# Optimization experiments

Measured on AMD Instinct MI355X. Metric: run time of the kernel, lower is better.

Reference implementation:

```python
import jax, jax.numpy as jnp
import numpy as np

BL = 512              # block length (init kwarg bl)
HALF = BL // 2
WIN = BL + 2 * HALF   # window width seen by each query block
Q_DIM = K_DIM = V_DIM = 256
R1 = R2 = R3 = 2
CQ, CK, CV = Q_DIM // R1, K_DIM // R2, V_DIM // R3


def setup_inputs() -> dict:
    key = jax.random.key(0)
    ks = jax.random.split(key, 9)
    B, L = 1, 131072
    def w(k, shape, fan):
        return (jax.random.normal(k, shape, jnp.float32) / np.float32(np.sqrt(fan)))
    return {
        "x1": jax.random.normal(ks[0], (B, Q_DIM, L), jnp.float32),
        "mask": jnp.ones((B, 1, L), jnp.float32),
        "Wq": w(ks[1], (CQ, Q_DIM), Q_DIM), "bq": jnp.zeros((CQ,), jnp.float32),
        "Wk": w(ks[2], (CK, K_DIM), K_DIM), "bk": jnp.zeros((CK,), jnp.float32),
        "Wv": w(ks[3], (CV, V_DIM), V_DIM), "bv": jnp.zeros((CV,), jnp.float32),
        "Wo": w(ks[4], (V_DIM, CV), CV),   "bo": jnp.zeros((V_DIM,), jnp.float32),
    }


def conv1x1(W, b, x):
    # nn.Conv1d(kernel_size=1): (B, Cin, L) -> (B, Cout, L)
    return jnp.einsum('oc,bcl->bol', W, x) + b[None, :, None]


def _sliding_window_att(q, k, v, mask):
    B, cq, L = q.shape
    cv = v.shape[1]
    nb = L // BL  # L chosen divisible by BL (remainder-pad branch is a no-op)
    # per-frame padding mask, (B,1,L)
    pm = jnp.broadcast_to(mask[:, 0:1, :], (B, 1, L))
    # blocked queries: (B*nb, cq, BL)
    qb = q.reshape(B, cq, nb, BL).transpose(0, 2, 1, 3).reshape(B * nb, cq, BL)
    # pad k / v / mask by HALF zeros on both sides, then take overlapping windows
    kp = jnp.pad(k, ((0, 0), (0, 0), (HALF, HALF)))
    vp = jnp.pad(v, ((0, 0), (0, 0), (HALF, HALF)))
    mp = jnp.pad(pm, ((0, 0), (0, 0), (HALF, HALF)))
    idx = np.arange(nb)[:, None] * BL + np.arange(WIN)[None, :]
    kb = kp[:, :, idx].transpose(0, 2, 1, 3).reshape(B * nb, -1, WIN)
    vb = vp[:, :, idx].transpose(0, 2, 1, 3).reshape(B * nb, -1, WIN)
    mb = mp[:, :, idx].transpose(0, 2, 1, 3).reshape(B * nb, 1, WIN)
    # construct_window_mask: loop sets window_mask[:, :, i:i+BL] = 1 for i in [0,BL),
    # whose union is columns [0, 2*BL-1) for ALL rows (faithful to the given code).
    wm = (jnp.arange(WIN) < (2 * BL - 1)).astype(q.dtype)[None, None, :]
    fm = wm * mb  # final mask, broadcasts over the BL query rows
    # scalar_dot_att with log-mask trick
    energy = jnp.einsum('ncl,ncw->nlw', qb, kb) / np.float32(np.sqrt(cq))
    att = jax.nn.softmax(energy + jnp.log(fm + 1e-6), axis=-1) * fm
    out = jnp.einsum('ncw,nlw->ncl', vb, att)  # (B*nb, cv, BL)
    return out, nb, cv


def reference(x1, mask, Wq, bq, Wk, bk, Wv, bv, Wo, bo):
    B, _, L = x1.shape
    q = conv1x1(Wq, bq, x1)
    k = conv1x1(Wk, bk, x1)
    v = conv1x1(Wv, bv, x1)
    out, nb, cv = _sliding_window_att(q, k, v, mask)
    out = conv1x1(Wo, bo, jax.nn.relu(out))  # (B*nb, V_DIM, BL)
    out = out.reshape(B, nb, V_DIM, BL).transpose(0, 2, 1, 3).reshape(B, V_DIM, nb * BL)
    out = out[:, :, :L]
    return out * mask[:, 0:1, :]
```

## Files before the change

kernel.cpp:

```cpp
#include <hip/hip_runtime.h>
#include <math.h>

#define LTOT 131072

typedef unsigned short u16;
typedef unsigned int   u32;
typedef __attribute__((ext_vector_type(8))) short bf16x8;
typedef __attribute__((ext_vector_type(4))) short bf16x4;
typedef __attribute__((ext_vector_type(4))) float f32x4;

__device__ __forceinline__ u16 f2b(float f) {
  union { float f; u32 u; } v; v.f = f;
  u32 r = v.u + 0x7fffu + ((v.u >> 16) & 1u);
  return (u16)(r >> 16);
}

__device__ __forceinline__ u32 cvt_pk(float lo, float hi) {
  u32 r;
  asm("v_cvt_pk_bf16_f32 %0, %1, %2" : "=v"(r) : "v"(lo), "v"(hi));
  return r;
}

__device__ __forceinline__ bf16x8 pack_bp(const f32x4 a, const f32x4 b) {
  union { u32 w[4]; bf16x8 v; } u;
  u.w[0] = cvt_pk(a[0], a[1]);
  u.w[1] = cvt_pk(a[2], a[3]);
  u.w[2] = cvt_pk(b[0], b[1]);
  u.w[3] = cvt_pk(b[2], b[3]);
  return u.v;
}

__device__ __forceinline__ int sxt_addr(int row, int g) {
  return (row << 8) + (((g) ^ (row & 7)) << 3);
}

__global__ __launch_bounds__(512) void k_qkv(
    const float* __restrict__ x1,
    const float* __restrict__ Wq, const float* __restrict__ bq,
    const float* __restrict__ Wk, const float* __restrict__ bk,
    const float* __restrict__ Wv, const float* __restrict__ bv,
    const float* __restrict__ Wo,
    u16* __restrict__ scratch, u16* __restrict__ WoB)
{
  __shared__ __align__(16) u16 sXT[128 * 256];

  const int tid  = threadIdx.x;
  const int lane = tid & 63;
  const int wv   = tid >> 6;
  const int lr   = lane & 15;
  const int lg   = lane >> 4;
  const int l0   = blockIdx.x << 7;

  {
    const int cl = (tid & 63) << 1;
    const int kq = tid >> 6;
#pragma unroll
    for (int k8 = 0; k8 < 4; ++k8) {
      const int k0 = kq * 32 + k8 * 8;
      float2 v[8];
#pragma unroll
      for (int j = 0; j < 8; ++j)
        v[j] = *reinterpret_cast<const float2*>(x1 + (size_t)(k0 + j) * LTOT + l0 + cl);
      union { u16 h[8]; bf16x8 b; } p0, p1;
#pragma unroll
      for (int j = 0; j < 8; ++j) {
        p0.h[j] = f2b(v[j].x);
        p1.h[j] = f2b(v[j].y);
      }
      const int g = k0 >> 3;
      *reinterpret_cast<bf16x8*>(&sXT[sxt_addr(cl,     g)]) = p0.b;
      *reinterpret_cast<bf16x8*>(&sXT[sxt_addr(cl + 1, g)]) = p1.b;
    }
  }

  if (blockIdx.x == 0) {
    for (int idx = tid; idx < 32768; idx += 512) WoB[idx] = f2b(Wo[idx]);
  }
  __syncthreads();

  const float rs = 0.1275174468f;

#pragma unroll
  for (int wb = 0; wb < 2; ++wb) {
    const float* Wsel = wb ? Wk : Wq;
    const float* bsel = wb ? bk : bq;
    const int c = (wv << 4) + lr;

    bf16x8 bw[8];
    {
      const float* wrow = Wsel + (size_t)c * 256 + (lg << 3);
#pragma unroll
      for (int kc = 0; kc < 8; ++kc) {
        float4 wa = *reinterpret_cast<const float4*>(wrow + kc * 32);
        float4 wc = *reinterpret_cast<const float4*>(wrow + kc * 32 + 4);
        union { u16 h[8]; bf16x8 b; } u;
        u.h[0] = f2b(wa.x); u.h[1] = f2b(wa.y); u.h[2] = f2b(wa.z); u.h[3] = f2b(wa.w);
        u.h[4] = f2b(wc.x); u.h[5] = f2b(wc.y); u.h[6] = f2b(wc.z); u.h[7] = f2b(wc.w);
        bw[kc] = u.b;
      }
    }

    f32x4 acc[8];
#pragma unroll
    for (int mt = 0; mt < 8; ++mt) acc[mt] = (f32x4){0.f, 0.f, 0.f, 0.f};
#pragma unroll
    for (int kc = 0; kc < 8; ++kc) {
      const int g = (kc << 2) + lg;
#pragma unroll
      for (int mt = 0; mt < 8; ++mt) {
        bf16x8 a = *reinterpret_cast<const bf16x8*>(&sXT[sxt_addr((mt << 4) + lr, g)]);
        acc[mt] = __builtin_amdgcn_mfma_f32_16x16x32_bf16(bw[kc], a, acc[mt], 0, 0, 0);
      }
    }

    const int c0 = (wv << 4) + (lg << 2);
    float4 b4 = *reinterpret_cast<const float4*>(bsel + c0);
    const float bb[4] = {b4.x, b4.y, b4.z, b4.w};
    const float scale = wb ? 1.f : rs;
    u16* dst = scratch + (size_t)wb * 128 * LTOT;
#pragma unroll
    for (int mt = 0; mt < 8; ++mt) {
      const int l = l0 + (mt << 4) + lr;
      union { u16 h[4]; uint2 v; } s;
#pragma unroll
      for (int r = 0; r < 4; ++r)
        s.h[r] = f2b((acc[mt][r] + bb[r]) * scale);
      *reinterpret_cast<uint2*>(dst + (size_t)l * 128 + c0) = s.v;
    }
  }

  {
    const int c = (wv << 4) + lr;
    bf16x8 aw[8];
    {
      const float* wrow = Wv + (size_t)c * 256 + (lg << 3);
#pragma unroll
      for (int kc = 0; kc < 8; ++kc) {
        float4 wa = *reinterpret_cast<const float4*>(wrow + kc * 32);
        float4 wc = *reinterpret_cast<const float4*>(wrow + kc * 32 + 4);
        union { u16 h[8]; bf16x8 b; } u;
        u.h[0] = f2b(wa.x); u.h[1] = f2b(wa.y); u.h[2] = f2b(wa.z); u.h[3] = f2b(wa.w);
        u.h[4] = f2b(wc.x); u.h[5] = f2b(wc.y); u.h[6] = f2b(wc.z); u.h[7] = f2b(wc.w);
        aw[kc] = u.b;
      }
    }

    f32x4 acc[8];
#pragma unroll
    for (int nt = 0; nt < 8; ++nt) acc[nt] = (f32x4){0.f, 0.f, 0.f, 0.f};
#pragma unroll
    for (int kc = 0; kc < 8; ++kc) {
      const int g = (kc << 2) + lg;
#pragma unroll
      for (int nt = 0; nt < 8; ++nt) {
        bf16x8 b = *reinterpret_cast<const bf16x8*>(&sXT[sxt_addr((nt << 4) + lr, g)]);
        acc[nt] = __builtin_amdgcn_mfma_f32_16x16x32_bf16(b, aw[kc], acc[nt], 0, 0, 0);
      }
    }

    const float bias = bv[c];
    u16* dstv = scratch + (size_t)256 * LTOT + (size_t)c * LTOT;
#pragma unroll
    for (int nt = 0; nt < 8; ++nt) {
      const int p0 = l0 + (nt << 4) + (lg << 2);
      union { u16 h[4]; uint2 v; } s;
#pragma unroll
      for (int r = 0; r < 4; ++r)
        s.h[r] = f2b(acc[nt][r] + bias);
      *reinterpret_cast<uint2*>(dstv + p0) = s.v;
    }
  }
}

__global__ __launch_bounds__(512, 4) void k_attn(
    const u16* __restrict__ scratch,
    const float* __restrict__ mask,
    u16* __restrict__ attT)
{
  __shared__ __align__(16) unsigned char smem[44032];
  u16*   sKT = (u16*)smem;
  u16*   sV  = (u16*)(smem + 17408);
  float* sLF = (float*)(smem + 35840);
  float* sFM = (float*)(smem + 39936);

  const int tid  = threadIdx.x;
  const int lane = tid & 63;
  const int wv   = tid >> 6;
  const int lr   = lane & 15;
  const int lg   = lane >> 4;
  const int lid  = ((int)blockIdx.x & 7) * 128 + ((int)blockIdx.x >> 3);
  const int lq0  = lid << 7;
  const int nblk = lq0 >> 9;
  const int p_base = nblk * 512 - 256;
  const int wq0  = lq0 + wv * 16;

  const u16* QT = scratch;
  const u16* KT = scratch + (size_t)128 * LTOT;
  const u16* Vp = scratch + (size_t)256 * LTOT;

  for (int idx = tid; idx < 1024; idx += 512) {
    int p = p_base + idx;
    float fmv = 0.f;
    if (idx < 1023 && (unsigned)p < (unsigned)LTOT) fmv = mask[p];
    sFM[idx] = fmv;
    sLF[idx] = log2f(fmv + 1e-6f);
  }

  bf16x8 aQ[4];
#pragma unroll
  for (int kc = 0; kc < 4; ++kc)
    aQ[kc] = *reinterpret_cast<const bf16x8*>(
        QT + (size_t)(wq0 + lr) * 128 + kc * 32 + (lg << 3));

  float m_run = -INFINITY;
  f32x4 d4 = (f32x4){0.f, 0.f, 0.f, 0.f};
  f32x4 accO[8];
#pragma unroll
  for (int cm = 0; cm < 8; ++cm) accO[cm] = (f32x4){0.f, 0.f, 0.f, 0.f};

  uint4 rk[2], rv[2];
  {
    const int p0 = p_base;
#pragma unroll
    for (int j = 0; j < 2; ++j) {
      int idx = tid + j * 512;
      int row = idx >> 4, ch = (idx & 15) << 3;
      int p = p0 + row;
      rk[j] = make_uint4(0u, 0u, 0u, 0u);
      if ((unsigned)p < (unsigned)LTOT)
        rk[j] = *reinterpret_cast<const uint4*>(KT + (size_t)p * 128 + ch);
      int c = idx >> 3, w = (idx & 7) << 3;
      int pp = p0 + w;
      rv[j] = make_uint4(0u, 0u, 0u, 0u);
      if ((unsigned)pp < (unsigned)LTOT)
        rv[j] = *reinterpret_cast<const uint4*>(Vp + (size_t)c * LTOT + pp);
    }
  }
#pragma unroll
  for (int j = 0; j < 2; ++j) {
    int idx = tid + j * 512;
    int row = idx >> 4, ch = (idx & 15) << 3;
    *reinterpret_cast<uint4*>(&sKT[row * 136 + ch]) = rk[j];
    int c = idx >> 3, w = (idx & 7) << 3;
    *reinterpret_cast<uint4*>(&sV[c * 72 + w]) = rv[j];
  }
  __syncthreads();

  for (int it = 0; it < 16; ++it) {
    if (it < 15) {
      const int p0 = p_base + (it + 1) * 64;
#pragma unroll
      for (int j = 0; j < 2; ++j) {
        int idx = tid + j * 512;
        int row = idx >> 4, ch = (idx & 15) << 3;
        int p = p0 + row;
        rk[j] = make_uint4(0u, 0u, 0u, 0u);
        if ((unsigned)p < (unsigned)LTOT)
          rk[j] = *reinterpret_cast<const uint4*>(KT + (size_t)p * 128 + ch);
        int c = idx >> 3, w = (idx & 7) << 3;
        int pp = p0 + w;
        rv[j] = make_uint4(0u, 0u, 0u, 0u);
        if ((unsigned)pp < (unsigned)LTOT)
          rv[j] = *reinterpret_cast<const uint4*>(Vp + (size_t)c * LTOT + pp);
      }
    }

    f32x4 e[4];
#pragma unroll
    for (int nt = 0; nt < 4; ++nt) e[nt] = (f32x4){0.f, 0.f, 0.f, 0.f};
#pragma unroll
    for (int kc = 0; kc < 4; ++kc) {
      const int ko = kc * 32 + (lg << 3);
#pragma unroll
      for (int nt = 0; nt < 4; ++nt) {
        bf16x8 bk = *reinterpret_cast<const bf16x8*>(&sKT[(nt * 16 + lr) * 136 + ko]);
        e[nt] = __builtin_amdgcn_mfma_f32_16x16x32_bf16(bk, aQ[kc], e[nt], 0, 0, 0);
      }
    }

    const int wbase = it * 64 + (lg << 2);
#pragma unroll
    for (int nt = 0; nt < 4; ++nt) {
      f32x4 lf = *reinterpret_cast<const f32x4*>(&sLF[wbase + nt * 16]);
      e[nt] += lf;
    }

    float lmax = e[0][0];
#pragma unroll
    for (int nt = 0; nt < 4; ++nt)
#pragma unroll
      for (int r = 0; r < 4; ++r) if (nt || r) lmax = fmaxf(lmax, e[nt][r]);

    if (__any(lmax > m_run + 12.0f)) {
      float rmax = lmax;
      rmax = fmaxf(rmax, __shfl_xor(rmax, 16));
      rmax = fmaxf(rmax, __shfl_xor(rmax, 32));
      float mnew = fmaxf(m_run, rmax);
      float fs = exp2f(m_run - mnew);
      d4 *= fs;
#pragma unroll
      for (int cm = 0; cm < 8; ++cm) accO[cm] *= fs;
      m_run = mnew;
    }

    f32x4 pn[4];
#pragma unroll
    for (int nt = 0; nt < 4; ++nt) {
      f32x4 fmv = *reinterpret_cast<const f32x4*>(&sFM[wbase + nt * 16]);
      f32x4 pd;
#pragma unroll
      for (int r = 0; r < 4; ++r) pd[r] = exp2f(e[nt][r] - m_run);
      d4 += pd;
      pn[nt] = pd * fmv;
    }
    bf16x8 bp0 = pack_bp(pn[0], pn[1]);
    bf16x8 bp1 = pack_bp(pn[2], pn[3]);

#pragma unroll
    for (int k2 = 0; k2 < 2; ++k2) {
      const bf16x8 bp = k2 ? bp1 : bp0;
      const int vo = k2 * 32 + (lg << 2);
#pragma unroll
      for (int cm = 0; cm < 8; ++cm) {
        const u16* vr = &sV[(cm * 16 + lr) * 72 + vo];
        bf16x4 v0 = *reinterpret_cast<const bf16x4*>(vr);
        bf16x4 v1 = *reinterpret_cast<const bf16x4*>(vr + 16);
        bf16x8 av = __builtin_shufflevector(v0, v1, 0, 1, 2, 3, 4, 5, 6, 7);
        accO[cm] = __builtin_amdgcn_mfma_f32_16x16x32_bf16(av, bp, accO[cm], 0, 0, 0);
      }
    }

    __syncthreads();
    if (it < 15) {
#pragma unroll
      for (int j = 0; j < 2; ++j) {
        int idx = tid + j * 512;
        int row = idx >> 4, ch = (idx & 15) << 3;
        *reinterpret_cast<uint4*>(&sKT[row * 136 + ch]) = rk[j];
        int c = idx >> 3, w = (idx & 7) << 3;
        *reinterpret_cast<uint4*>(&sV[c * 72 + w]) = rv[j];
      }
    }
    __syncthreads();
  }

  float dsum = d4[0] + d4[1] + d4[2] + d4[3];
  dsum += __shfl_xor(dsum, 16);
  dsum += __shfl_xor(dsum, 32);
  const float rd = 1.f / dsum;

  __syncthreads();
  u16* sT = (u16*)smem + wv * 2176;
#pragma unroll
  for (int cm = 0; cm < 8; ++cm) {
    float o0 = fmaxf(accO[cm][0] * rd, 0.f);
    float o1 = fmaxf(accO[cm][1] * rd, 0.f);
    float o2 = fmaxf(accO[cm][2] * rd, 0.f);
    float o3 = fmaxf(accO[cm][3] * rd, 0.f);
    uint2 pk = make_uint2(cvt_pk(o0, o1), cvt_pk(o2, o3));
    *reinterpret_cast<uint2*>(&sT[lr * 136 + cm * 16 + (lg << 2)]) = pk;
  }
  __syncthreads();
  for (int idx = lane; idx < 256; idx += 64) {
    int row = idx >> 4, ch = (idx & 15) << 3;
    uint4 v = *reinterpret_cast<const uint4*>(&sT[row * 136 + ch]);
    *reinterpret_cast<uint4*>(attT + (size_t)(wq0 + row) * 128 + ch) = v;
  }
}

__device__ __forceinline__ int sa_addr(int row, int g) {
  return (row << 7) + (((g) ^ (row & 7)) << 3);
}

__global__ __launch_bounds__(512) void k_out(
    const u16* __restrict__ attT, const u16* __restrict__ WoB,
    const float* __restrict__ bo, const float* __restrict__ mask,
    float* __restrict__ out)
{
  __shared__ __align__(16) u16 sA[128 * 128];

  const int tid  = threadIdx.x;
  const int lane = tid & 63;
  const int wv   = tid >> 6;
  const int lr   = lane & 15;
  const int lg   = lane >> 4;
  const int l0   = blockIdx.x << 7;

  for (int idx = tid; idx < 2048; idx += 512) {
    int row = idx >> 4, g = idx & 15;
    uint4 v = *reinterpret_cast<const uint4*>(attT + (size_t)(l0 + row) * 128 + (g << 3));
    *reinterpret_cast<uint4*>(&sA[sa_addr(row, g)]) = v;
  }
  __syncthreads();

  const int ob = wv << 5;
  f32x4 acc[2][8];
#pragma unroll
  for (int mt = 0; mt < 2; ++mt)
#pragma unroll
    for (int nt = 0; nt < 8; ++nt) acc[mt][nt] = (f32x4){0.f, 0.f, 0.f, 0.f};

#pragma unroll
  for (int kc = 0; kc < 4; ++kc) {
    bf16x8 a[2], b[8];
#pragma unroll
    for (int mt = 0; mt < 2; ++mt)
      a[mt] = *reinterpret_cast<const bf16x8*>(
          WoB + (size_t)(ob + mt * 16 + lr) * 128 + kc * 32 + (lg << 3));
    const int g = (kc << 2) + lg;
#pragma unroll
    for (int nt = 0; nt < 8; ++nt)
      b[nt] = *reinterpret_cast<const bf16x8*>(&sA[sa_addr(nt * 16 + lr, g)]);
#pragma unroll
    for (int mt = 0; mt < 2; ++mt)
#pragma unroll
      for (int nt = 0; nt < 8; ++nt)
        acc[mt][nt] = __builtin_amdgcn_mfma_f32_16x16x32_bf16(a[mt], b[nt], acc[mt][nt], 0, 0, 0);
  }

#pragma unroll
  for (int mt = 0; mt < 2; ++mt) {
    const int o0 = ob + mt * 16 + (lg << 2);
    float4 b4 = *reinterpret_cast<const float4*>(bo + o0);
#pragma unroll
    for (int nt = 0; nt < 8; ++nt) {
      const int l = l0 + nt * 16 + lr;
      const float mk = mask[l];
      out[(size_t)(o0 + 0) * LTOT + l] = (acc[mt][nt][0] + b4.x) * mk;
      out[(size_t)(o0 + 1) * LTOT + l] = (acc[mt][nt][1] + b4.y) * mk;
      out[(size_t)(o0 + 2) * LTOT + l] = (acc[mt][nt][2] + b4.z) * mk;
      out[(size_t)(o0 + 3) * LTOT + l] = (acc[mt][nt][3] + b4.w) * mk;
    }
  }
}

extern "C" void kernel_launch(void* const* d_in, const int* in_sizes, int n_in,
                              void* d_out, int out_size, void* d_ws, size_t ws_size,
                              hipStream_t stream) {
  (void)in_sizes; (void)n_in; (void)out_size; (void)ws_size;
  const float* x1   = (const float*)d_in[0];
  const float* mask = (const float*)d_in[1];
  const float* Wq   = (const float*)d_in[2];
  const float* bq   = (const float*)d_in[3];
  const float* Wk   = (const float*)d_in[4];
  const float* bk   = (const float*)d_in[5];
  const float* Wv   = (const float*)d_in[6];
  const float* bv   = (const float*)d_in[7];
  const float* Wo   = (const float*)d_in[8];
  const float* bo   = (const float*)d_in[9];

  u16* scratch = (u16*)d_out;
  u16* attT    = (u16*)d_ws;
  u16* WoB     = attT + (size_t)128 * LTOT;
  float* out   = (float*)d_out;

  hipLaunchKernelGGL(k_qkv, dim3(1024), dim3(512), 0, stream,
                     x1, Wq, bq, Wk, bk, Wv, bv, Wo, scratch, WoB);
  hipLaunchKernelGGL(k_attn, dim3(1024), dim3(512), 0, stream,
                     scratch, mask, attT);
  hipLaunchKernelGGL(k_out, dim3(1024), dim3(512), 0, stream,
                     attT, WoB, bo, mask, out);
}
```

Measured before the change: 250.6 us.

## Process two query tiles per wave in attention to reuse K/V LDS fragments

Halves the attention block to 256 threads (4 waves) and has each wave compute two 16-row query tiles, 32 rows in all, with separate online-softmax state per tile. Each K and V fragment read from LDS now feeds two MFMAs instead of one, which cuts LDS read traffic per unit of matrix work. It also drops two block-wide barriers in the epilogue, since each wave only touches its own staging area. In exchange each thread holds roughly twice the accumulator and Q registers, and fewer waves are resident per CU to hide latency.

```diff
diff --git a/kernel.cpp b/kernel.cpp
--- a/kernel.cpp
+++ b/kernel.cpp
@@ -172,7 +172,7 @@
   }
 }
 
-__global__ __launch_bounds__(512, 4) void k_attn(
+__global__ __launch_bounds__(256, 2) void k_attn(
     const u16* __restrict__ scratch,
     const float* __restrict__ mask,
     u16* __restrict__ attT)
@@ -190,15 +190,14 @@
   const int lg   = lane >> 4;
   const int lid  = ((int)blockIdx.x & 7) * 128 + ((int)blockIdx.x >> 3);
   const int lq0  = lid << 7;
-  const int nblk = lq0 >> 9;
-  const int p_base = nblk * 512 - 256;
-  const int wq0  = lq0 + wv * 16;
+  const int p_base = (lq0 >> 9) * 512 - 256;
+  const int wq0  = lq0 + wv * 32;
 
   const u16* QT = scratch;
   const u16* KT = scratch + (size_t)128 * LTOT;
   const u16* Vp = scratch + (size_t)256 * LTOT;
 
-  for (int idx = tid; idx < 1024; idx += 512) {
+  for (int idx = tid; idx < 1024; idx += 256) {
     int p = p_base + idx;
     float fmv = 0.f;
     if (idx < 1023 && (unsigned)p < (unsigned)LTOT) fmv = mask[p];
@@ -206,24 +205,31 @@
     sLF[idx] = log2f(fmv + 1e-6f);
   }
 
-  bf16x8 aQ[4];
-#pragma unroll
-  for (int kc = 0; kc < 4; ++kc)
-    aQ[kc] = *reinterpret_cast<const bf16x8*>(
+  bf16x8 aQ0[4], aQ1[4];
+#pragma unroll
+  for (int kc = 0; kc < 4; ++kc) {
+    aQ0[kc] = *reinterpret_cast<const bf16x8*>(
         QT + (size_t)(wq0 + lr) * 128 + kc * 32 + (lg << 3));
-
-  float m_run = -INFINITY;
-  f32x4 d4 = (f32x4){0.f, 0.f, 0.f, 0.f};
-  f32x4 accO[8];
-#pragma unroll
-  for (int cm = 0; cm < 8; ++cm) accO[cm] = (f32x4){0.f, 0.f, 0.f, 0.f};
-
-  uint4 rk[2], rv[2];
+    aQ1[kc] = *reinterpret_cast<const bf16x8*>(
+        QT + (size_t)(wq0 + 16 + lr) * 128 + kc * 32 + (lg << 3));
+  }
+
+  float m0 = -INFINITY, m1 = -INFINITY;
+  f32x4 d40 = (f32x4){0.f, 0.f, 0.f, 0.f};
+  f32x4 d41 = (f32x4){0.f, 0.f, 0.f, 0.f};
+  f32x4 accO0[8], accO1[8];
+#pragma unroll
+  for (int cm = 0; cm < 8; ++cm) {
+    accO0[cm] = (f32x4){0.f, 0.f, 0.f, 0.f};
+    accO1[cm] = (f32x4){0.f, 0.f, 0.f, 0.f};
+  }
+
+  uint4 rk[4], rv[4];
   {
     const int p0 = p_base;
 #pragma unroll
-    for (int j = 0; j < 2; ++j) {
-      int idx = tid + j * 512;
+    for (int j = 0; j < 4; ++j) {
+      int idx = tid + j * 256;
       int row = idx >> 4, ch = (idx & 15) << 3;
       int p = p0 + row;
       rk[j] = make_uint4(0u, 0u, 0u, 0u);
@@ -237,8 +243,8 @@
     }
   }
 #pragma unroll
-  for (int j = 0; j < 2; ++j) {
-    int idx = tid + j * 512;
+  for (int j = 0; j < 4; ++j) {
+    int idx = tid + j * 256;
     int row = idx >> 4, ch = (idx & 15) << 3;
     *reinterpret_cast<uint4*>(&sKT[row * 136 + ch]) = rk[j];
     int c = idx >> 3, w = (idx & 7) << 3;
@@ -250,8 +256,8 @@
     if (it < 15) {
       const int p0 = p_base + (it + 1) * 64;
 #pragma unroll
-      for (int j = 0; j < 2; ++j) {
-        int idx = tid + j * 512;
+      for (int j = 0; j < 4; ++j) {
+        int idx = tid + j * 256;
         int row = idx >> 4, ch = (idx & 15) << 3;
         int p = p0 + row;
         rk[j] = make_uint4(0u, 0u, 0u, 0u);
@@ -265,60 +271,99 @@
       }
     }
 
-    f32x4 e[4];
-#pragma unroll
-    for (int nt = 0; nt < 4; ++nt) e[nt] = (f32x4){0.f, 0.f, 0.f, 0.f};
+    f32x4 e0[4], e1[4];
+#pragma unroll
+    for (int nt = 0; nt < 4; ++nt) {
+      e0[nt] = (f32x4){0.f, 0.f, 0.f, 0.f};
+      e1[nt] = (f32x4){0.f, 0.f, 0.f, 0.f};
+    }
 #pragma unroll
     for (int kc = 0; kc < 4; ++kc) {
       const int ko = kc * 32 + (lg << 3);
 #pragma unroll
       for (int nt = 0; nt < 4; ++nt) {
         bf16x8 bk = *reinterpret_cast<const bf16x8*>(&sKT[(nt * 16 + lr) * 136 + ko]);
-        e[nt] = __builtin_amdgcn_mfma_f32_16x16x32_bf16(bk, aQ[kc], e[nt], 0, 0, 0);
+        e0[nt] = __builtin_amdgcn_mfma_f32_16x16x32_bf16(bk, aQ0[kc], e0[nt], 0, 0, 0);
+        e1[nt] = __builtin_amdgcn_mfma_f32_16x16x32_bf16(bk, aQ1[kc], e1[nt], 0, 0, 0);
       }
     }
 
     const int wbase = it * 64 + (lg << 2);
+    f32x4 lf[4], fmv[4];
 #pragma unroll
     for (int nt = 0; nt < 4; ++nt) {
-      f32x4 lf = *reinterpret_cast<const f32x4*>(&sLF[wbase + nt * 16]);
-      e[nt] += lf;
-    }
-
-    float lmax = e[0][0];
-#pragma unroll
-    for (int nt = 0; nt < 4; ++nt)
-#pragma unroll
-      for (int r = 0; r < 4; ++r) if (nt || r) lmax = fmaxf(lmax, e[nt][r]);
-
-    if (__any(lmax > m_run + 12.0f)) {
-      float rmax = lmax;
-      rmax = fmaxf(rmax, __shfl_xor(rmax, 16));
-      rmax = fmaxf(rmax, __shfl_xor(rmax, 32));
-      float mnew = fmaxf(m_run, rmax);
-      float fs = exp2f(m_run - mnew);
-      d4 *= fs;
-#pragma unroll
-      for (int cm = 0; cm < 8; ++cm) accO[cm] *= fs;
-      m_run = mnew;
-    }
-
-    f32x4 pn[4];
-#pragma unroll
-    for (int nt = 0; nt < 4; ++nt) {
-      f32x4 fmv = *reinterpret_cast<const f32x4*>(&sFM[wbase + nt * 16]);
-      f32x4 pd;
-#pragma unroll
-      for (int r = 0; r < 4; ++r) pd[r] = exp2f(e[nt][r] - m_run);
-      d4 += pd;
-      pn[nt] = pd * fmv;
-    }
-    bf16x8 bp0 = pack_bp(pn[0], pn[1]);
-    bf16x8 bp1 = pack_bp(pn[2], pn[3]);
+      lf[nt]  = *reinterpret_cast<const f32x4*>(&sLF[wbase + nt * 16]);
+      fmv[nt] = *reinterpret_cast<const f32x4*>(&sFM[wbase + nt * 16]);
+      e0[nt] += lf[nt];
+      e1[nt] += lf[nt];
+    }
+
+    bf16x8 bpA0, bpA1;
+    {
+      float lmax = e0[0][0];
+#pragma unroll
+      for (int nt = 0; nt < 4; ++nt)
+#pragma unroll
+        for (int r = 0; r < 4; ++r) if (nt || r) lmax = fmaxf(lmax, e0[nt][r]);
+      if (__any(lmax > m0 + 12.0f)) {
+        float rmax = lmax;
+        rmax = fmaxf(rmax, __shfl_xor(rmax, 16));
+        rmax = fmaxf(rmax, __shfl_xor(rmax, 32));
+        float mnew = fmaxf(m0, rmax);
+        float fs = exp2f(m0 - mnew);
+        d40 *= fs;
+#pragma unroll
+        for (int cm = 0; cm < 8; ++cm) accO0[cm] *= fs;
+        m0 = mnew;
+      }
+      f32x4 pn[4];
+#pragma unroll
+      for (int nt = 0; nt < 4; ++nt) {
+        f32x4 pd;
+#pragma unroll
+        for (int r = 0; r < 4; ++r) pd[r] = exp2f(e0[nt][r] - m0);
+        d40 += pd;
+        pn[nt] = pd * fmv[nt];
+      }
+      bpA0 = pack_bp(pn[0], pn[1]);
+      bpA1 = pack_bp(pn[2], pn[3]);
+    }
+
+    bf16x8 bpB0, bpB1;
+    {
+      float lmax = e1[0][0];
+#pragma unroll
+      for (int nt = 0; nt < 4; ++nt)
+#pragma unroll
+        for (int r = 0; r < 4; ++r) if (nt || r) lmax = fmaxf(lmax, e1[nt][r]);
+      if (__any(lmax > m1 + 12.0f)) {
+        float rmax = lmax;
+        rmax = fmaxf(rmax, __shfl_xor(rmax, 16));
+        rmax = fmaxf(rmax, __shfl_xor(rmax, 32));
+        float mnew = fmaxf(m1, rmax);
+        float fs = exp2f(m1 - mnew);
+        d41 *= fs;
+#pragma unroll
+        for (int cm = 0; cm < 8; ++cm) accO1[cm] *= fs;
+        m1 = mnew;
+      }
+      f32x4 pn[4];
+#pragma unroll
+      for (int nt = 0; nt < 4; ++nt) {
+        f32x4 pd;
+#pragma unroll
+        for (int r = 0; r < 4; ++r) pd[r] = exp2f(e1[nt][r] - m1);
+        d41 += pd;
+        pn[nt] = pd * fmv[nt];
+      }
+      bpB0 = pack_bp(pn[0], pn[1]);
+      bpB1 = pack_bp(pn[2], pn[3]);
+    }
 
 #pragma unroll
     for (int k2 = 0; k2 < 2; ++k2) {
-      const bf16x8 bp = k2 ? bp1 : bp0;
+      const bf16x8 pA = k2 ? bpA1 : bpA0;
+      const bf16x8 pB = k2 ? bpB1 : bpB0;
       const int vo = k2 * 32 + (lg << 2);
 #pragma unroll
       for (int cm = 0; cm < 8; ++cm) {
@@ -326,15 +371,16 @@
         bf16x4 v0 = *reinterpret_cast<const bf16x4*>(vr);
         bf16x4 v1 = *reinterpret_cast<const bf16x4*>(vr + 16);
         bf16x8 av = __builtin_shufflevector(v0, v1, 0, 1, 2, 3, 4, 5, 6, 7);
-        accO[cm] = __builtin_amdgcn_mfma_f32_16x16x32_bf16(av, bp, accO[cm], 0, 0, 0);
+        accO0[cm] = __builtin_amdgcn_mfma_f32_16x16x32_bf16(av, pA, accO0[cm], 0, 0, 0);
+        accO1[cm] = __builtin_amdgcn_mfma_f32_16x16x32_bf16(av, pB, accO1[cm], 0, 0, 0);
       }
     }
 
     __syncthreads();
     if (it < 15) {
 #pragma unroll
-      for (int j = 0; j < 2; ++j) {
-        int idx = tid + j * 512;
+      for (int j = 0; j < 4; ++j) {
+        int idx = tid + j * 256;
         int row = idx >> 4, ch = (idx & 15) << 3;
         *reinterpret_cast<uint4*>(&sKT[row * 136 + ch]) = rk[j];
         int c = idx >> 3, w = (idx & 7) << 3;
@@ -344,27 +390,43 @@
     __syncthreads();
   }
 
-  float dsum = d4[0] + d4[1] + d4[2] + d4[3];
-  dsum += __shfl_xor(dsum, 16);
-  dsum += __shfl_xor(dsum, 32);
-  const float rd = 1.f / dsum;
-
-  __syncthreads();
+  float ds0 = d40[0] + d40[1] + d40[2] + d40[3];
+  ds0 += __shfl_xor(ds0, 16);
+  ds0 += __shfl_xor(ds0, 32);
+  const float rd0 = 1.f / ds0;
+  float ds1 = d41[0] + d41[1] + d41[2] + d41[3];
+  ds1 += __shfl_xor(ds1, 16);
+  ds1 += __shfl_xor(ds1, 32);
+  const float rd1 = 1.f / ds1;
+
   u16* sT = (u16*)smem + wv * 2176;
 #pragma unroll
   for (int cm = 0; cm < 8; ++cm) {
-    float o0 = fmaxf(accO[cm][0] * rd, 0.f);
-    float o1 = fmaxf(accO[cm][1] * rd, 0.f);
-    float o2 = fmaxf(accO[cm][2] * rd, 0.f);
-    float o3 = fmaxf(accO[cm][3] * rd, 0.f);
+    float o0 = fmaxf(accO0[cm][0] * rd0, 0.f);
+    float o1 = fmaxf(accO0[cm][1] * rd0, 0.f);
+    float o2 = fmaxf(accO0[cm][2] * rd0, 0.f);
+    float o3 = fmaxf(accO0[cm][3] * rd0, 0.f);
     uint2 pk = make_uint2(cvt_pk(o0, o1), cvt_pk(o2, o3));
     *reinterpret_cast<uint2*>(&sT[lr * 136 + cm * 16 + (lg << 2)]) = pk;
   }
-  __syncthreads();
   for (int idx = lane; idx < 256; idx += 64) {
     int row = idx >> 4, ch = (idx & 15) << 3;
     uint4 v = *reinterpret_cast<const uint4*>(&sT[row * 136 + ch]);
     *reinterpret_cast<uint4*>(attT + (size_t)(wq0 + row) * 128 + ch) = v;
+  }
+#pragma unroll
+  for (int cm = 0; cm < 8; ++cm) {
+    float o0 = fmaxf(accO1[cm][0] * rd1, 0.f);
+    float o1 = fmaxf(accO1[cm][1] * rd1, 0.f);
+    float o2 = fmaxf(accO1[cm][2] * rd1, 0.f);
+    float o3 = fmaxf(accO1[cm][3] * rd1, 0.f);
+    uint2 pk = make_uint2(cvt_pk(o0, o1), cvt_pk(o2, o3));
+    *reinterpret_cast<uint2*>(&sT[lr * 136 + cm * 16 + (lg << 2)]) = pk;
+  }
+  for (int idx = lane; idx < 256; idx += 64) {
+    int row = idx >> 4, ch = (idx & 15) << 3;
+    uint4 v = *reinterpret_cast<const uint4*>(&sT[row * 136 + ch]);
+    *reinterpret_cast<uint4*>(attT + (size_t)(wq0 + 16 + row) * 128 + ch) = v;
   }
 }
 
@@ -456,7 +518,7 @@
 
   hipLaunchKernelGGL(k_qkv, dim3(1024), dim3(512), 0, stream,
                      x1, Wq, bq, Wk, bk, Wv, bv, Wo, scratch, WoB);
-  hipLaunchKernelGGL(k_attn, dim3(1024), dim3(512), 0, stream,
+  hipLaunchKernelGGL(k_attn, dim3(1024), dim3(256), 0, stream,
                      scratch, mask, attT);
   hipLaunchKernelGGL(k_out, dim3(1024), dim3(512), 0, stream,
                      attT, WoB, bo, mask, out);
```

Result: faster. 228.4 us (-8.9%).
